# Optimization experiments

Hardware: AMD Instinct MI355X
Metric: run time of the kernel (lower is better)

Reference implementation:

```python
import jax, jax.numpy as jnp
import numpy as np
from jax.scipy.special import i0

# NUFFT adjoint (gridding) configuration, matching m_op.plan(uv, (256,256), (512,512), (6,6))
N = 256          # image side
K = 512
J = 6            # kernel support per dim
B = 8            # batch
M = 100000       # n_measurements
ALPHA = K / N    # oversampling = 2
BETA = float(np.pi * np.sqrt((J / ALPHA * (ALPHA - 0.5)) ** 2 - 0.8))  # Fessler KB beta


def setup_inputs() -> dict:
    key = jax.random.key(0)
    k1, k2, k3, k4 = jax.random.split(key, 4)
    y_real = jax.random.normal(k1, (B, M), dtype=jnp.float32)
    y_imag = jax.random.normal(k2, (B, M), dtype=jnp.float32)
    weights = jax.random.uniform(k3, (M,), dtype=jnp.float32, minval=0.1, maxval=1.0)
    uv = jax.random.uniform(k4, (M, 2), dtype=jnp.float32,
                            minval=-np.pi, maxval=np.pi)
    return {"y_real": y_real, "y_imag": y_imag, "weights": weights, "uv": uv}


def _kb(t):
    # Kaiser-Bessel interpolation kernel, support |t| <= J/2
    u = 2.0 * t / J
    return i0(BETA * jnp.sqrt(jnp.clip(1.0 - u * u, 0.0))) / i0(jnp.asarray(BETA, jnp.float32))


def reference(y_real, y_imag, weights, uv):
    # weighted complex measurements: inputs * measurement_weights
    y = (y_real + 1j * y_imag) * weights[None, :]           # (B, M) complex64

    # map uv in [-pi, pi) to oversampled grid coords in [0, K)
    kf = uv * (K / (2.0 * np.pi))                            # (M, 2), DC at index 0 (mod K)
    base = jnp.floor(kf).astype(jnp.int32)                   # (M, 2)
    offs = jnp.arange(-J // 2 + 1, J // 2 + 1)               # [-2..3], 6 taps
    idx = base[:, :, None] + offs[None, None, :]             # (M, 2, J)
    dist = idx.astype(jnp.float32) - kf[:, :, None]
    w = _kb(dist)                                            # (M, 2, J) separable weights
    idxm = jnp.mod(idx, K)                                   # wrap onto torus

    w2 = (w[:, 0, :, None] * w[:, 1, None, :]).reshape(M, J * J)          # (M, 36)
    lin = (idxm[:, 0, :, None] * K + idxm[:, 1, None, :]).reshape(M * J * J)
    vals = (y[:, :, None] * w2[None, :, :].astype(jnp.complex64)).reshape(B, M * J * J)

    # scatter-add onto oversampled Fourier grid
    grid = jnp.zeros((B, K * K), jnp.complex64).at[:, lin].add(vals)
    grid = grid.reshape(B, K, K)

    # inverse FFT, center, crop to N x N
    img = jnp.fft.fftshift(jnp.fft.ifft2(grid), axes=(1, 2))
    c = K // 2
    img = img[:, c - N // 2:c + N // 2, c - N // 2:c + N // 2]

    # deapodization: divide by 1D FT of the KB kernel (always real here since BETA > pi*J/4*... )
    n = jnp.arange(N, dtype=jnp.float32) - N // 2
    xf = np.pi * J * n / K
    arg = BETA * BETA - xf * xf
    d = jnp.sinh(jnp.sqrt(arg)) / jnp.sqrt(arg)              # (N,)
    apod = d[:, None] * d[None, :]

    x = (jnp.real(img) / apod).astype(jnp.float32)           # tf.math.real(adj_op(...))

    # per-image min-max rescale
    tmax = jnp.max(x, axis=(1, 2), keepdims=True)
    tmin = jnp.min(x, axis=(1, 2), keepdims=True)
    return (x - tmin) / (tmax - tmin)
```

## Files before the change

kernel.cpp:

```cpp
#include <hip/hip_runtime.h>
#include <math.h>

#define NN 256
#define KK 512
#define JJ 6
#define BB 8
#define MPTS 100000
#define NBINS (KK * KK)
#define KF_SCALE 81.48733086305615f

typedef _Float16 h8 __attribute__((ext_vector_type(8)));


__device__ __forceinline__ float i0f_dev(float x) {
    float ax = fabsf(x);
    if (ax < 3.75f) {
        float t = x / 3.75f; t *= t;
        return 1.0f + t*(3.5156229f + t*(3.0899424f + t*(1.2067492f +
               t*(0.2659732f + t*(0.0360768f + t*0.0045813f)))));
    } else {
        float t = 3.75f / ax;
        return (expf(ax) * rsqrtf(ax)) *
               (0.39894228f + t*(0.01328592f + t*(0.00225319f + t*(-0.00157565f +
                t*(0.00916281f + t*(-0.02057706f + t*(0.02635537f +
                t*(-0.01647633f + t*0.00392377f))))))));
    }
}

__device__ __forceinline__ float kbf(float t, float beta, float inv_i0b) {
    float u = t * (1.0f / 3.0f);
    float q = fmaxf(1.0f - u * u, 0.0f);
    return i0f_dev(beta * sqrtf(q)) * inv_i0b;
}

__device__ __forceinline__ int wave_scan(int x, int lane) {
#pragma unroll
    for (int off = 1; off < 64; off <<= 1) {
        int y = __shfl_up(x, off, 64);
        if (lane >= off) x += y;
    }
    return x;
}

__device__ __forceinline__ float kb_lut(const float* __restrict__ sT, float t) {
    float u = (t + 3.0f) * (1023.0f / 6.0f);
    int i = (int)u;
    i = min(i, 1022);
    float f = u - (float)i;
    float a = sT[i];
    return a + f * (sT[i + 1] - sT[i]);
}


__global__ __launch_bounds__(256) void count_bins(
    const float2* __restrict__ uv2, int* __restrict__ counts,
    float* __restrict__ lut, float beta, float inv_i0b)
{
    int m = blockIdx.x * 256 + threadIdx.x;
    if (m < 1024) {
        float t = -3.0f + (6.0f / 1023.0f) * (float)m;
        lut[m] = kbf(t, beta, inv_i0b);
    }
    if (m >= MPTS) return;
    float2 u = uv2[m];
    int b0 = (int)floorf(u.x * KF_SCALE) & (KK - 1);
    int b1 = (int)floorf(u.y * KF_SCALE) & (KK - 1);
    atomicAdd(&counts[(b0 << 9) | b1], 1);
}

__global__ __launch_bounds__(1024) void scan_k(
    const int* __restrict__ counts, int* __restrict__ offsets,
    unsigned long long* __restrict__ desc)
{
    __shared__ int part[16];
    __shared__ int s_prefix;
    int tid = threadIdx.x;
    int lane = tid & 63;
    int w = tid >> 6;
    int g = blockIdx.x * 1024 + tid;

    int v = counts[g];
    int x = wave_scan(v, lane);
    if (lane == 63) part[w] = x;
    __syncthreads();
    if (tid < 16) {
        int p = part[tid];
#pragma unroll
        for (int off = 1; off < 16; off <<= 1) {
            int y = __shfl_up(p, off, 64);
            if (tid >= off) p += y;
        }
        part[tid] = p;
    }
    __syncthreads();
    int incl = x + ((w > 0) ? part[w - 1] : 0);
    int total = part[15];

    if (tid == 0) {
        unsigned long long pack = ((unsigned long long)(unsigned)total << 2) |
                                  ((blockIdx.x == 0) ? 2ULL : 1ULL);
        atomicExch(&desc[blockIdx.x], pack);
        if (blockIdx.x == 0) s_prefix = 0;
    }

    if (blockIdx.x > 0 && w == 0) {
        int prefix = 0;
        int base = blockIdx.x - 1;
        bool done = false;
        while (!done) {
            int idx = base - lane;
            unsigned long long d = 0;
            if (idx >= 0) {
                do { d = atomicAdd(&desc[idx], 0ULL); } while ((d & 3ULL) == 0ULL);
            }
            unsigned long long mask = __ballot(idx >= 0 && (d & 3ULL) == 2ULL);
            int f = (mask != 0ULL) ? (__ffsll((long long)mask) - 1) : 64;
            int contrib = (idx >= 0 && lane <= f) ? (int)(d >> 2) : 0;
#pragma unroll
            for (int off = 1; off < 64; off <<= 1)
                contrib += __shfl_xor(contrib, off, 64);
            prefix += contrib;
            base -= 64;
            done = (mask != 0ULL);
        }
        if (lane == 0) {
            s_prefix = prefix;
            atomicExch(&desc[blockIdx.x],
                       ((unsigned long long)(unsigned)(prefix + total) << 2) | 2ULL);
        }
    }
    __syncthreads();

    offsets[g] = incl - v + s_prefix;
    if (g == 0) offsets[NBINS] = MPTS;
}

__global__ __launch_bounds__(256) void fill_records(
    const float2* __restrict__ uv2,
    const float* __restrict__ y_real, const float* __restrict__ y_imag,
    const float* __restrict__ weights, const int* __restrict__ offsets,
    int* __restrict__ counts, char* __restrict__ rec,
    const float* __restrict__ lut)
{
    __shared__ float sT[1024];
    int tid = threadIdx.x;
#pragma unroll
    for (int q = 0; q < 4; ++q) sT[q * 256 + tid] = lut[q * 256 + tid];
    __syncthreads();

    int m = blockIdx.x * 256 + tid;
    if (m >= MPTS) return;
    float2 u = uv2[m];
    float kf0 = u.x * KF_SCALE;
    float kf1 = u.y * KF_SCALE;
    float f0 = floorf(kf0), f1 = floorf(kf1);
    float fr0 = kf0 - f0, fr1 = kf1 - f1;
    int b1c = (int)f1 & (KK - 1);
    int bin = (((int)f0 & (KK - 1)) << 9) | b1c;
    int old = atomicSub(&counts[bin], 1);
    int slot = offsets[bin] + old - 1;

    _Float16 hw[12];
#pragma unroll
    for (int j = 0; j < JJ; ++j) {
        hw[j]     = (_Float16)kb_lut(sT, (float)(j - 2) - fr0);
        hw[6 + j] = (_Float16)kb_lut(sT, (float)(j - 2) - fr1);
    }

    float4 c0v, c1v;
    _Float16* p0 = (_Float16*)&c0v;
    _Float16* p1 = (_Float16*)&c1v;
#pragma unroll
    for (int j = 0; j < 8; ++j) p0[j] = hw[j];
#pragma unroll
    for (int j = 0; j < 4; ++j) p1[j] = hw[8 + j];
    ((int*)&c1v)[2] = b1c;
    ((int*)&c1v)[3] = 0;

    float wm = weights[m];
    h8 ha, hb;
#pragma unroll
    for (int b = 0; b < 4; ++b) {
        ha[2 * b]     = (_Float16)(y_real[b * MPTS + m] * wm);
        ha[2 * b + 1] = (_Float16)(y_imag[b * MPTS + m] * wm);
        hb[2 * b]     = (_Float16)(y_real[(b + 4) * MPTS + m] * wm);
        hb[2 * b + 1] = (_Float16)(y_imag[(b + 4) * MPTS + m] * wm);
    }

    float4* dst = (float4*)(rec + (size_t)slot * 64);
    dst[0] = c0v;
    dst[1] = c1v;
    dst[2] = *(float4*)&ha;
    dst[3] = *(float4*)&hb;
}

__global__ __launch_bounds__(256) void gather_grid(
    const int* __restrict__ offsets, const char* __restrict__ rec,
    float* __restrict__ grid)
{
    __shared__ __align__(16) char lds[4][2816];
    int t = threadIdx.x;
    int lane = t & 63;
    int w = t >> 6;
    int half = lane >> 5;
    int l32 = lane & 31;
    int j = blockIdx.x;
    int xcd = j & 7;
    int c0 = (xcd << 6) + ((j >> 3) & 63);
    int q4 = j >> 9;
    int c1base = (q4 << 7) + (w << 5);
    int c1 = c1base + l32;
    int wa = c1 - 3, wb = c1 + 2;

    char* myl = lds[w];

    float aR[4], aI[4];
#pragma unroll
    for (int b = 0; b < 4; ++b) { aR[b] = 0.0f; aI[b] = 0.0f; }

    for (int j0 = 0; j0 < JJ; ++j0) {
        int r0 = (c0 - (j0 - 2)) & (KK - 1);
        int rowbase = r0 << 9;
        int lo = c1base - 3, hi = c1base + 33;
        int nseg, ga0, gb0, ga1, gb1;
        if (lo < 0)        { ga0 = lo; gb0 = -1;  ga1 = 0;   gb1 = hi; nseg = 2; }
        else if (hi > 511) { ga0 = lo; gb0 = 511; ga1 = 512; gb1 = hi; nseg = 2; }
        else               { ga0 = lo; gb0 = hi;  ga1 = 0;   gb1 = 0;  nseg = 1; }

        for (int sgi = 0; sgi < nseg; ++sgi) {
            int ga = sgi ? ga1 : ga0;
            int gb = sgi ? gb1 : gb0;
            int pstart = offsets[rowbase + (ga & 511)];
            int pend   = offsets[rowbase + ((gb & 511) + 1)];
            int ia = max(wa, ga), ib = min(wb, gb);
            bool has = ia <= ib;
            int pA = has ? offsets[rowbase + (ia & 511)] : 0;
            int pB = has ? ((ib == gb) ? pend
                                       : offsets[rowbase + ((ib + 1) & 511)]) : 0;

            for (int pc = pstart; pc < pend; pc += 32) {
                int cnt = min(32, pend - pc);
                int sub = lane & 3;
                int prow = lane >> 2;
#pragma unroll
                for (int qq = 0; qq < 2; ++qq) {
                    if (16 * qq < cnt) {
                        int pp = min(pc + prow + 16 * qq, MPTS - 1);
                        float4 v = *(const float4*)(rec + (size_t)pp * 64 + sub * 16);
                        *(float4*)(myl + (prow + 16 * qq) * 88 + sub * 16) = v;
                    }
                }
                int pLo = max(pA, pc), pHi = min(pB, pc + cnt);
                for (int p = pLo; p < pHi; ++p) {
                    const char* rp = myl + (p - pc) * 88;
                    int bin1 = *(const int*)(rp + 24);
                    int idx = (c1 - bin1 + 2) & 511;
                    bool ok = idx <= 5;
                    idx = ok ? idx : 0;
                    float w0 = (float)*(const _Float16*)(rp + j0 * 2);
                    float w1 = (float)*(const _Float16*)(rp + 12 + idx * 2);
                    float ww = ok ? w0 * w1 : 0.0f;
                    h8 yv = *(const h8*)(rp + 32 + (half << 4));
#pragma unroll
                    for (int b = 0; b < 4; ++b) {
                        aR[b] += (float)yv[2 * b]     * ww;
                        aI[b] += (float)yv[2 * b + 1] * ww;
                    }
                }
            }
        }
    }

    float2* g2 = (float2*)grid;
    int c = (c0 << 9) + c1;
#pragma unroll
    for (int b = 0; b < 4; ++b)
        g2[((size_t)((half << 2) + b) << 18) + c] = make_float2(aR[b], aI[b]);
}

__device__ __forceinline__ void wave_fft512(float xr[8], float xi[8], int lane,
                                            const float2* __restrict__ tw)
{
    float a0r = xr[0]+xr[4], a0i = xi[0]+xi[4];
    float a4r = xr[0]-xr[4], a4i = xi[0]-xi[4];
    float a2r = xr[2]+xr[6], a2i = xi[2]+xi[6];
    float a6r = xr[2]-xr[6], a6i = xi[2]-xi[6];
    float a1r = xr[1]+xr[5], a1i = xi[1]+xi[5];
    float a5r = xr[1]-xr[5], a5i = xi[1]-xi[5];
    float a3r = xr[3]+xr[7], a3i = xi[3]+xi[7];
    float a7r = xr[3]-xr[7], a7i = xi[3]-xi[7];
    float b0r = a0r+a2r, b0i = a0i+a2i;
    float b2r = a0r-a2r, b2i = a0i-a2i;
    float b4r = a4r-a6i, b4i = a4i+a6r;
    float b6r = a4r+a6i, b6i = a4i-a6r;
    float b1r = a1r+a3r, b1i = a1i+a3i;
    float b3r = a1r-a3r, b3i = a1i-a3i;
    float b5r = a5r-a7i, b5i = a5i+a7r;
    float b7r = a5r+a7i, b7i = a5i-a7r;
    const float S2 = 0.70710678118654752f;
    float w5r = S2*(b5r-b5i), w5i = S2*(b5r+b5i);
    float w7r = -S2*(b7r+b7i), w7i = S2*(b7r-b7i);
    float y0r = b0r+b1r, y0i = b0i+b1i;
    float y4r = b0r-b1r, y4i = b0i-b1i;
    float y1r = b4r+w5r, y1i = b4i+w5i;
    float y5r = b4r-w5r, y5i = b4i-w5i;
    float y2r = b2r-b3i, y2i = b2i+b3r;
    float y6r = b2r+b3i, y6i = b2i-b3r;
    float y3r = b6r+w7r, y3i = b6i+w7i;
    float y7r = b6r-w7r, y7i = b6i-w7i;

    int p = __brev((unsigned)lane) >> 26;
    float2 w0v = tw[p];
    float c1 = w0v.x, s1 = w0v.y;
    float wr = c1, wi = s1, tr;
    xr[0] = y0r; xi[0] = y0i;
    xr[1] = y1r*wr - y1i*wi; xi[1] = y1i*wr + y1r*wi;
    tr = wr*c1 - wi*s1; wi = wr*s1 + wi*c1; wr = tr;
    xr[2] = y2r*wr - y2i*wi; xi[2] = y2i*wr + y2r*wi;
    tr = wr*c1 - wi*s1; wi = wr*s1 + wi*c1; wr = tr;
    xr[3] = y3r*wr - y3i*wi; xi[3] = y3i*wr + y3r*wi;
    tr = wr*c1 - wi*s1; wi = wr*s1 + wi*c1; wr = tr;
    xr[4] = y4r*wr - y4i*wi; xi[4] = y4i*wr + y4r*wi;
    tr = wr*c1 - wi*s1; wi = wr*s1 + wi*c1; wr = tr;
    xr[5] = y5r*wr - y5i*wi; xi[5] = y5i*wr + y5r*wi;
    tr = wr*c1 - wi*s1; wi = wr*s1 + wi*c1; wr = tr;
    xr[6] = y6r*wr - y6i*wi; xi[6] = y6i*wr + y6r*wi;
    tr = wr*c1 - wi*s1; wi = wr*s1 + wi*c1; wr = tr;
    xr[7] = y7r*wr - y7i*wi; xi[7] = y7i*wr + y7r*wi;

#pragma unroll
    for (int t = 0; t < 6; ++t) {
        int m = 1 << t;
        int j = lane & (m - 1);
        float wc, wsn;
        sincosf((float)M_PI * (float)j / (float)m, &wsn, &wc);
        bool hi = (lane & m) != 0;
#pragma unroll
        for (int d = 0; d < 8; ++d) {
            float pR = __shfl_xor(xr[d], m, 64);
            float pI = __shfl_xor(xi[d], m, 64);
            float bR = hi ? xr[d] : pR;
            float bI = hi ? xi[d] : pI;
            float aR = hi ? pR : xr[d];
            float aI = hi ? pI : xi[d];
            float wbR = wc * bR - wsn * bI;
            float wbI = wc * bI + wsn * bR;
            xr[d] = hi ? aR - wbR : aR + wbR;
            xi[d] = hi ? aI - wbI : aI + wbI;
        }
    }
}

__global__ __launch_bounds__(512) void fftA(
    const float2* __restrict__ grid2, float2* __restrict__ C)
{
    __shared__ float sR[2112], sI[2112];
    __shared__ float2 tw[256];
    int t = threadIdx.x;
    int lane = t & 63;
    int w = t >> 6;
    int b = blockIdx.x & 7;
    int k1base = (blockIdx.x >> 3) << 3;
    int k1 = k1base + w;

    if (t < 256) {
        float ang = (float)(2.0 * M_PI / 512.0) * (float)t;
        float s, c; sincosf(ang, &s, &c);
        tw[t] = make_float2(c, s);
    }

    const float2* row = grid2 + ((size_t)b << 18) + ((size_t)k1 << 9);
    int p = __brev((unsigned)lane) >> 26;
    float xr[8], xi[8];
#pragma unroll
    for (int a = 0; a < 8; ++a) {
        float2 v = row[p + (a << 6)];
        xr[a] = v.x; xi[a] = v.y;
    }
    __syncthreads();

    wave_fft512(xr, xi, lane, tw);

    bool act = (lane < 16) | (lane >= 48);
    int lpp = (lane < 16) ? lane : (lane - 32);
    if (act) {
#pragma unroll
        for (int d = 0; d < 8; ++d) {
            int addr = w * 264 + d * 33 + lpp;
            sR[addr] = xr[d];
            sI[addr] = xi[d];
        }
    }
    __syncthreads();

#pragma unroll
    for (int pp = 0; pp < 4; ++pp) {
        int idx = pp * 512 + t;
        int kk = idx & 7;
        int s2 = idx >> 3;
        int v = (s2 + 128) & 255;
        int d = v & 7;
        int lp = v >> 3;
        int addr = kk * 264 + d * 33 + lp;
        C[(((size_t)(b << 8) + s2) << 9) + k1base + kk] = make_float2(sR[addr], sI[addr]);
    }
}

__global__ __launch_bounds__(256) void fftB(
    const float2* __restrict__ C, float* __restrict__ imgT, float beta2,
    float* __restrict__ pmin, float* __restrict__ pmax)
{
    __shared__ float2 tw[256];
    __shared__ float invd[256];
    __shared__ float wmn[4], wmx[4];
    int t = threadIdx.x;
    int lane = t & 63;
    int w = t >> 6;
    int rowid = blockIdx.x * 4 + w;
    int b = rowid >> 8;
    int s2 = rowid & 255;

    {
        float ang = (float)(2.0 * M_PI / 512.0) * (float)t;
        float s, c; sincosf(ang, &s, &c);
        tw[t] = make_float2(c, s);
        const float XF = (float)(M_PI * (double)JJ / (double)KK);
        float n = (float)(t - 128);
        float xf = XF * n;
        float arg = beta2 - xf * xf;
        float sq = sqrtf(arg);
        invd[t] = sq / sinhf(sq);
    }

    const float2* row = C + ((size_t)rowid << 9);
    int p = __brev((unsigned)lane) >> 26;
    float xr[8], xi[8];
#pragma unroll
    for (int a = 0; a < 8; ++a) {
        float2 v = row[p + (a << 6)];
        xr[a] = v.x; xi[a] = v.y;
    }
    __syncthreads();

    wave_fft512(xr, xi, lane, tw);

    const float INVK2 = 1.0f / ((float)KK * (float)KK);
    float sbase = INVK2 * invd[s2];

    bool act = (lane < 16) | (lane >= 48);
    int lpp = (lane < 16) ? lane : (lane - 32);
    float lmin = 1e30f, lmax = -1e30f;
    if (act) {
        float vals[8];
#pragma unroll
        for (int d = 0; d < 8; ++d) {
            int r = (8 * lpp + d + 128) & 255;
            float o = xr[d] * sbase * invd[r];
            vals[d] = o;
            lmin = fminf(lmin, o);
            lmax = fmaxf(lmax, o);
        }
        int r0run = (8 * lpp + 128) & 255;
        float4* dst = (float4*)(imgT + ((size_t)b << 16) + (s2 << 8) + r0run);
        dst[0] = make_float4(vals[0], vals[1], vals[2], vals[3]);
        dst[1] = make_float4(vals[4], vals[5], vals[6], vals[7]);
    }
#pragma unroll
    for (int off = 32; off >= 1; off >>= 1) {
        lmin = fminf(lmin, __shfl_xor(lmin, off, 64));
        lmax = fmaxf(lmax, __shfl_xor(lmax, off, 64));
    }
    if (lane == 0) { wmn[w] = lmin; wmx[w] = lmax; }
    __syncthreads();
    if (t == 0) {
        float mn = fminf(fminf(wmn[0], wmn[1]), fminf(wmn[2], wmn[3]));
        float mx = fmaxf(fmaxf(wmx[0], wmx[1]), fmaxf(wmx[2], wmx[3]));
        pmin[blockIdx.x] = mn;
        pmax[blockIdx.x] = mx;
    }
}

__global__ __launch_bounds__(256) void norm_t(
    const float* __restrict__ imgT, const float* __restrict__ pmin,
    const float* __restrict__ pmax, float* __restrict__ out)
{
    __shared__ float tile[64][65];
    __shared__ float s_mn, s_inv;
    int b = blockIdx.x >> 4;
    int tl = blockIdx.x & 15;
    int r0 = (tl & 3) << 6;
    int s0 = (tl >> 2) << 6;
    int tr = threadIdx.x & 63;
    int ts = threadIdx.x >> 6;

    if (threadIdx.x < 64) {
        float mn = pmin[(b << 6) + threadIdx.x];
        float mx = pmax[(b << 6) + threadIdx.x];
#pragma unroll
        for (int off = 32; off >= 1; off >>= 1) {
            mn = fminf(mn, __shfl_xor(mn, off, 64));
            mx = fmaxf(mx, __shfl_xor(mx, off, 64));
        }
        if (threadIdx.x == 0) { s_mn = mn; s_inv = 1.0f / (mx - mn); }
    }

    const float* src = imgT + ((size_t)b << 16);
#pragma unroll
    for (int q = 0; q < 16; ++q) {
        int s2 = s0 + (q << 2) + ts;
        tile[s2 - s0][tr] = src[(s2 << 8) + r0 + tr];
    }
    __syncthreads();

    float mn = s_mn, inv = s_inv;
    float* dst = out + ((size_t)b << 16);
#pragma unroll
    for (int q = 0; q < 16; ++q) {
        int r = r0 + (q << 2) + ts;
        dst[(r << 8) + s0 + tr] = (tile[tr][r - r0] - mn) * inv;
    }
}


static double i0_host(double x) {
    double sum = 1.0, term = 1.0;
    double q = x * x * 0.25;
    for (int k = 1; k < 80; ++k) {
        term *= q / ((double)k * (double)k);
        sum += term;
        if (term < sum * 1e-17) break;
    }
    return sum;
}

extern "C" void kernel_launch(void* const* d_in, const int* in_sizes, int n_in,
                              void* d_out, int out_size, void* d_ws, size_t ws_size,
                              hipStream_t stream)
{
    const float* y_real  = (const float*)d_in[0];
    const float* y_imag  = (const float*)d_in[1];
    const float* weights = (const float*)d_in[2];
    const float2* uv2    = (const float2*)d_in[3];
    float* out = (float*)d_out;

    char* W = (char*)d_ws;
    float*    grid    = (float*)W;
    int*      counts  = (int*)W;
    unsigned long long* desc = (unsigned long long*)(W + 0x100000);
    float*    imgT    = (float*)W;
    char*     A       = W + (size_t)16 * 1024 * 1024;
    char*     rec     = A;
    int*      offsets = (int*)(A + 6400000);
    float2*   C       = (float2*)A;
    float*    pmin    = (float*)(A + 8400000);
    float*    pmax    = (float*)(A + 8402048);
    float*    lut     = (float*)(A + 8404096);

    double beta_d = M_PI * sqrt(19.45);
    float beta = (float)beta_d;
    float inv_i0b = (float)(1.0 / i0_host(beta_d));
    float beta2 = (float)(beta_d * beta_d);

    hipMemsetAsync(counts, 0, NBINS * sizeof(int) + 256 * sizeof(unsigned long long),
                   stream);

    count_bins<<<(MPTS + 255) / 256, 256, 0, stream>>>(
        uv2, counts, lut, beta, inv_i0b);

    scan_k<<<256, 1024, 0, stream>>>(counts, offsets, desc);

    fill_records<<<(MPTS + 255) / 256, 256, 0, stream>>>(
        uv2, y_real, y_imag, weights, offsets, counts, rec, lut);

    gather_grid<<<2048, 256, 0, stream>>>(offsets, rec, grid);

    fftA<<<512, 512, 0, stream>>>((const float2*)grid, C);

    fftB<<<512, 256, 0, stream>>>(C, imgT, beta2, pmin, pmax);

    norm_t<<<128, 256, 0, stream>>>(imgT, pmin, pmax, out);
}
```

Before: 148.3 us.

## Split fftB row FFT into even/odd 256-point FFTs across two waves

The second-pass 512-point FFT is now computed as two 256-point FFTs, on the even and odd samples, by two waves per row. The final radix-2 butterfly combines them through shared memory and computes only the real outputs the crop needs. This doubles the threads per row and halves the registers and shuffle work per wave, to improve latency and occupancy, at the cost of an extra barrier and shared-memory exchange. fftA's block-to-row mapping is also reordered, interleaving batches and row groups, likely for memory locality.

```diff
diff --git a/kernel.cpp b/kernel.cpp
--- a/kernel.cpp
+++ b/kernel.cpp
@@ -351,6 +351,52 @@
     }
 }
 
+__device__ __forceinline__ void wave_fft256(float xr[4], float xi[4], int lane,
+                                            const float2* __restrict__ tw)
+{
+    float t0r = xr[0]+xr[2], t0i = xi[0]+xi[2];
+    float t1r = xr[0]-xr[2], t1i = xi[0]-xi[2];
+    float t2r = xr[1]+xr[3], t2i = xi[1]+xi[3];
+    float t3r = xr[1]-xr[3], t3i = xi[1]-xi[3];
+    float y0r = t0r+t2r, y0i = t0i+t2i;
+    float y2r = t0r-t2r, y2i = t0i-t2i;
+    float y1r = t1r-t3i, y1i = t1i+t3r;
+    float y3r = t1r+t3i, y3i = t1i-t3r;
+
+    int p = __brev((unsigned)lane) >> 26;
+    float2 wv = tw[p << 1];
+    float c1 = wv.x, s1 = wv.y;
+    float wr = c1, wi = s1, tr;
+    xr[0] = y0r; xi[0] = y0i;
+    xr[1] = y1r*wr - y1i*wi; xi[1] = y1i*wr + y1r*wi;
+    tr = wr*c1 - wi*s1; wi = wr*s1 + wi*c1; wr = tr;
+    xr[2] = y2r*wr - y2i*wi; xi[2] = y2i*wr + y2r*wi;
+    tr = wr*c1 - wi*s1; wi = wr*s1 + wi*c1; wr = tr;
+    xr[3] = y3r*wr - y3i*wi; xi[3] = y3i*wr + y3r*wi;
+
+#pragma unroll
+    for (int t = 0; t < 6; ++t) {
+        int m = 1 << t;
+        int j = lane & (m - 1);
+        float wc, wsn;
+        sincosf((float)M_PI * (float)j / (float)m, &wsn, &wc);
+        bool hi = (lane & m) != 0;
+#pragma unroll
+        for (int d = 0; d < 4; ++d) {
+            float pR = __shfl_xor(xr[d], m, 64);
+            float pI = __shfl_xor(xi[d], m, 64);
+            float bR = hi ? xr[d] : pR;
+            float bI = hi ? xi[d] : pI;
+            float aR = hi ? pR : xr[d];
+            float aI = hi ? pI : xi[d];
+            float wbR = wc * bR - wsn * bI;
+            float wbI = wc * bI + wsn * bR;
+            xr[d] = hi ? aR - wbR : aR + wbR;
+            xi[d] = hi ? aI - wbI : aI + wbI;
+        }
+    }
+}
+
 __global__ __launch_bounds__(512) void fftA(
     const float2* __restrict__ grid2, float2* __restrict__ C)
 {
@@ -359,8 +405,9 @@
     int t = threadIdx.x;
     int lane = t & 63;
     int w = t >> 6;
-    int b = blockIdx.x & 7;
-    int k1base = (blockIdx.x >> 3) << 3;
+    int x  = blockIdx.x & 7;
+    int b  = (blockIdx.x >> 3) & 7;
+    int k1base = (x << 6) | (((blockIdx.x >> 6) & 7) << 3);
     int k1 = k1base + w;
 
     if (t < 256) {
@@ -406,71 +453,89 @@
     }
 }
 
-__global__ __launch_bounds__(256) void fftB(
+__global__ __launch_bounds__(512) void fftB(
     const float2* __restrict__ C, float* __restrict__ imgT, float beta2,
     float* __restrict__ pmin, float* __restrict__ pmax)
 {
     __shared__ float2 tw[256];
     __shared__ float invd[256];
+    __shared__ __align__(16) float wor[4][256];
     __shared__ float wmn[4], wmx[4];
     int t = threadIdx.x;
     int lane = t & 63;
     int w = t >> 6;
-    int rowid = blockIdx.x * 4 + w;
+    int row = w >> 1;
+    int odd = w & 1;
+    int rowid = blockIdx.x * 4 + row;
     int b = rowid >> 8;
     int s2 = rowid & 255;
 
-    {
+    if (t < 256) {
         float ang = (float)(2.0 * M_PI / 512.0) * (float)t;
         float s, c; sincosf(ang, &s, &c);
         tw[t] = make_float2(c, s);
+    } else if (t < 512) {
+        int i = t - 256;
         const float XF = (float)(M_PI * (double)JJ / (double)KK);
-        float n = (float)(t - 128);
+        float n = (float)(i - 128);
         float xf = XF * n;
         float arg = beta2 - xf * xf;
         float sq = sqrtf(arg);
-        invd[t] = sq / sinhf(sq);
-    }
-
-    const float2* row = C + ((size_t)rowid << 9);
+        invd[i] = sq / sinhf(sq);
+    }
+
+    const float2* rowp = C + ((size_t)rowid << 9);
     int p = __brev((unsigned)lane) >> 26;
-    float xr[8], xi[8];
-#pragma unroll
-    for (int a = 0; a < 8; ++a) {
-        float2 v = row[p + (a << 6)];
+    float xr[4], xi[4];
+#pragma unroll
+    for (int a = 0; a < 4; ++a) {
+        float2 v = rowp[((p + (a << 6)) << 1) | odd];
         xr[a] = v.x; xi[a] = v.y;
     }
     __syncthreads();
 
-    wave_fft512(xr, xi, lane, tw);
-
-    const float INVK2 = 1.0f / ((float)KK * (float)KK);
-    float sbase = INVK2 * invd[s2];
-
-    bool act = (lane < 16) | (lane >= 48);
-    int lpp = (lane < 16) ? lane : (lane - 32);
-    float lmin = 1e30f, lmax = -1e30f;
-    if (act) {
-        float vals[8];
-#pragma unroll
-        for (int d = 0; d < 8; ++d) {
-            int r = (8 * lpp + d + 128) & 255;
-            float o = xr[d] * sbase * invd[r];
+    wave_fft256(xr, xi, lane, tw);
+
+    if (odd) {
+        float4 wo;
+#pragma unroll
+        for (int d = 0; d < 4; ++d) {
+            int k = (lane << 2) + d;
+            float2 wv = tw[k];
+            ((float*)&wo)[d] = xr[d] * wv.x - xi[d] * wv.y;
+        }
+        *(float4*)&wor[row][lane << 2] = wo;
+    }
+    __syncthreads();
+
+    if (!odd) {
+        const float INVK2 = 1.0f / ((float)KK * (float)KK);
+        float sbase = INVK2 * invd[s2];
+        float lmin = 1e30f, lmax = -1e30f;
+        float4 wo = *(const float4*)&wor[row][lane << 2];
+        float vals[4];
+#pragma unroll
+        for (int d = 0; d < 4; ++d) {
+            int k = (lane << 2) + d;
+            float e = xr[d];
+            float woK = ((const float*)&wo)[d];
+            float xre = (k < 128) ? (e + woK) : (e - woK);
+            int r = (k + 128) & 255;
+            float o = xre * sbase * invd[r];
             vals[d] = o;
             lmin = fminf(lmin, o);
             lmax = fmaxf(lmax, o);
         }
-        int r0run = (8 * lpp + 128) & 255;
-        float4* dst = (float4*)(imgT + ((size_t)b << 16) + (s2 << 8) + r0run);
-        dst[0] = make_float4(vals[0], vals[1], vals[2], vals[3]);
-        dst[1] = make_float4(vals[4], vals[5], vals[6], vals[7]);
-    }
-#pragma unroll
-    for (int off = 32; off >= 1; off >>= 1) {
-        lmin = fminf(lmin, __shfl_xor(lmin, off, 64));
-        lmax = fmaxf(lmax, __shfl_xor(lmax, off, 64));
-    }
-    if (lane == 0) { wmn[w] = lmin; wmx[w] = lmax; }
+        int r0run = ((lane << 2) + 128) & 255;
+        *(float4*)(imgT + ((size_t)b << 16) + (s2 << 8) + r0run) =
+            make_float4(vals[0], vals[1], vals[2], vals[3]);
+#pragma unroll
+        for (int off = 32; off >= 1; off >>= 1) {
+            lmin = fminf(lmin, __shfl_xor(lmin, off, 64));
+            lmax = fmaxf(lmax, __shfl_xor(lmax, off, 64));
+        }
+        if (lane == 0) { wmn[row] = lmin; wmx[row] = lmax; }
+    }
     __syncthreads();
     if (t == 0) {
         float mn = fminf(fminf(wmn[0], wmn[1]), fminf(wmn[2], wmn[3]));
@@ -576,7 +641,7 @@
 
     fftA<<<512, 512, 0, stream>>>((const float2*)grid, C);
 
-    fftB<<<512, 256, 0, stream>>>(C, imgT, beta2, pmin, pmax);
+    fftB<<<512, 512, 0, stream>>>(C, imgT, beta2, pmin, pmax);
 
     norm_t<<<128, 256, 0, stream>>>(imgT, pmin, pmax, out);
 }
```

Result: faster. 142.1 us (-4.2%).
